# Kernel optimization log

Measured on AMD Instinct MI355X. Metric: run time of the kernel, lower is better.

The kernel has to match this reference:

```python
import jax, jax.numpy as jnp
import numpy as np

HID = 256      # cfg.MODEL.YOSO.HIDDEN_DIM
NPROP = 100    # cfg.MODEL.YOSO.NUM_PROPOSALS
K1 = 3         # CONV_KERNEL_SIZE_1D
K2 = 1         # CONV_KERNEL_SIZE_2D
NCLS = 80      # NUM_CLASSES
NHEAD = 8

def layernorm(x, g, b, eps=1e-5):
    m = jnp.mean(x, -1, keepdims=True)
    v = jnp.var(x, -1, keepdims=True)
    return (x - m) * jax.lax.rsqrt(v + eps) * g + b

def dysep(query, value, Wl, bl, ng, nb):
    # dynamic depthwise conv (kernel K1 along feature axis, one kernel per proposal)
    # followed by dynamic pointwise NxN conv, per torch F.conv1d semantics (cross-correlation, 'same' pad)
    w = query @ Wl + bl                      # [B,N,N+K1]
    dw = w[..., :K1]                         # [B,N,K1] depthwise kernels
    pw = w[..., K1:]                         # [B,N,N]  pointwise mixing
    C = value.shape[-1]
    pad = K1 // 2
    vp = jnp.pad(value, ((0, 0), (0, 0), (pad, pad)))
    depth = sum(dw[..., k:k + 1] * vp[..., k:k + C] for k in range(K1))
    depth = jax.nn.relu(depth)
    point = jnp.einsum('bmn,bnc->bmc', pw, depth)
    return layernorm(point, ng, nb)

def mha(x, in_w, in_b, out_w, out_b):
    B, N, E = x.shape
    d = E // NHEAD
    qkv = x @ in_w + in_b
    q, k, v = jnp.split(qkv, 3, axis=-1)
    q = q.reshape(B, N, NHEAD, d)
    k = k.reshape(B, N, NHEAD, d)
    v = v.reshape(B, N, NHEAD, d)
    att = jnp.einsum('bqhd,bkhd->bhqk', q, k) / jnp.sqrt(jnp.asarray(d, x.dtype))
    att = jax.nn.softmax(att, axis=-1)
    o = jnp.einsum('bhqk,bkhd->bqhd', att, v).reshape(B, N, E)
    return o @ out_w + out_b

def setup_inputs() -> dict:
    key = jax.random.key(0)
    ks = iter(jax.random.split(key, 64))
    B, H, W = 8, 128, 128
    E = HID * K2 * K2
    nrm = lambda *s: jax.random.normal(next(ks), s, jnp.float32) * 0.02
    bias_value = -np.log((1 - 0.01) / 0.01)
    return dict(
        features=jax.random.normal(next(ks), (B, HID, H, W), jnp.float32),
        proposal_kernels=jax.random.normal(next(ks), (B, NPROP, E), jnp.float32),
        mask_preds=jax.random.normal(next(ks), (B, NPROP, H, W), jnp.float32),
        fW=nrm(E, NPROP + K1), fb=jnp.zeros(NPROP + K1), fng=jnp.ones(E), fnb=jnp.zeros(E),
        f_norm_g=jnp.ones(E), f_norm_b=jnp.zeros(E),
        kW=nrm(E, NPROP + K1), kb=jnp.zeros(NPROP + K1), kng=jnp.ones(E), knb=jnp.zeros(E),
        k_norm_g=jnp.ones(E), k_norm_b=jnp.zeros(E),
        attn_in_w=nrm(E, 3 * E), attn_in_b=jnp.zeros(3 * E),
        attn_out_w=nrm(E, E), attn_out_b=jnp.zeros(E),
        s_norm_g=jnp.ones(E), s_norm_b=jnp.zeros(E),
        ffn_w1=nrm(HID, 2048), ffn_b1=jnp.zeros(2048),
        ffn_w2=nrm(2048, HID), ffn_b2=jnp.zeros(HID),
        ffn_norm_g=jnp.ones(HID), ffn_norm_b=jnp.zeros(HID),
        cls_w=nrm(HID, HID), cls_ln_g=jnp.ones(HID), cls_ln_b=jnp.zeros(HID),
        fc_cls_w=nrm(HID, NCLS + 1), fc_cls_b=jnp.full((NCLS + 1,), bias_value, jnp.float32),
        mask_w=nrm(3, HID, HID), mask_ln_g=jnp.ones((3, HID)), mask_ln_b=jnp.zeros((3, HID)),
        fc_mask_w=nrm(HID, HID), fc_mask_b=jnp.zeros(HID),
        train_flag=1,
    )

def reference(features, proposal_kernels, mask_preds, fW, fb, fng, fnb, f_norm_g, f_norm_b,
              kW, kb, kng, knb, k_norm_g, k_norm_b,
              attn_in_w, attn_in_b, attn_out_w, attn_out_b, s_norm_g, s_norm_b,
              ffn_w1, ffn_b1, ffn_w2, ffn_b2, ffn_norm_g, ffn_norm_b,
              cls_w, cls_ln_g, cls_ln_b, fc_cls_w, fc_cls_b,
              mask_w, mask_ln_g, mask_ln_b, fc_mask_w, fc_mask_b, train_flag):
    B, C, H, W = features.shape
    hard = (jax.nn.sigmoid(mask_preds) > 0.5).astype(features.dtype)   # hard masks (no grad path)
    f = jnp.einsum('bnhw,bchw->bnc', hard, features)                   # mask-pooled features [B,N,E]
    k = proposal_kernels.reshape(B, NPROP, -1)
    f = layernorm(f + dysep(k, f, fW, fb, fng, fnb), f_norm_g, f_norm_b)
    kk = layernorm(f + dysep(k, f, kW, kb, kng, knb), k_norm_g, k_norm_b)
    kk = layernorm(kk + mha(kk, attn_in_w, attn_in_b, attn_out_w, attn_out_b), s_norm_g, s_norm_b)
    obj = jnp.transpose(kk.reshape(B, NPROP, HID, -1), (0, 1, 3, 2))   # [B,N,K2*K2,HID]
    h = jax.nn.relu(obj @ ffn_w1 + ffn_b1)
    obj = layernorm(obj + (h @ ffn_w2 + ffn_b2), ffn_norm_g, ffn_norm_b)
    cls_feat = obj.sum(-2)                                             # [B,N,HID]
    mask_feat = obj
    if train_flag:
        cls_feat = jax.nn.relu(layernorm(cls_feat @ cls_w, cls_ln_g, cls_ln_b))
        cls_score = (cls_feat @ fc_cls_w + fc_cls_b).reshape(B, NPROP, -1)
    else:
        cls_score = None
    for i in range(mask_w.shape[0]):
        mask_feat = jax.nn.relu(layernorm(mask_feat @ mask_w[i], mask_ln_g[i], mask_ln_b[i]))
    mask_kernels = (mask_feat @ fc_mask_w + fc_mask_b)[:, :, 0, :]     # squeeze(2), K2*K2==1
    new_mask_preds = jnp.einsum('bqc,bchw->bqhw', mask_kernels, features)
    obj_out = jnp.transpose(obj, (0, 1, 3, 2)).reshape(B, NPROP, HID, K2, K2)
    return (cls_score, new_mask_preds, obj_out)
```

## Files before the change

kernel.cpp:

```cpp
#include <hip/hip_runtime.h>

typedef float f32x4 __attribute__((ext_vector_type(4)));
typedef short bfrag __attribute__((ext_vector_type(8)));
typedef short sh4 __attribute__((ext_vector_type(4)));

__device__ __forceinline__ unsigned short f2bf(float x) {
  unsigned int u = __float_as_uint(x);
  return (unsigned short)((u + 0x7FFFu + ((u >> 16) & 1u)) >> 16);
}
__device__ __forceinline__ float bf2f(unsigned short u) {
  return __uint_as_float(((unsigned int)u) << 16);
}
__device__ __forceinline__ float wred_sum(float v) {
#pragma unroll
  for (int o = 32; o > 0; o >>= 1) v += __shfl_xor(v, o);
  return v;
}
__device__ __forceinline__ float wred_max(float v) {
#pragma unroll
  for (int o = 32; o > 0; o >>= 1) v = fmaxf(v, __shfl_xor(v, o));
  return v;
}

struct Prep12 {
  const float* s[12];
  int K[12];
  int N[12];
  int base[12];
  int doff[12];
};

__global__ __launch_bounds__(256) void prep_w(Prep12 p, unsigned short* wt) {
  int t = blockIdx.x;
  int wi = 0;
#pragma unroll
  for (int i = 0; i < 11; ++i)
    if (t >= p.base[i + 1]) wi = i + 1;
  int lt = t - p.base[wi];
  int K = p.K[wi], N = p.N[wi];
  int tkn = (K + 31) >> 5;
  int tk = lt % tkn, tn = lt / tkn;
  __shared__ float tile[32][33];
  const float* src = p.s[wi];
#pragma unroll
  for (int i = 0; i < 4; ++i) {
    int flat = i * 256 + threadIdx.x;
    int kl = flat >> 5, nl = flat & 31;
    int k = tk * 32 + kl, n = tn * 32 + nl;
    tile[kl][nl] = (k < K && n < N) ? src[(size_t)k * N + n] : 0.f;
  }
  __syncthreads();
  unsigned short* dst = wt + p.doff[wi];
#pragma unroll
  for (int i = 0; i < 4; ++i) {
    int flat = i * 256 + threadIdx.x;
    int nl = flat >> 5, kl = flat & 31;
    int k = tk * 32 + kl, n = tn * 32 + nl;
    if (k < K && n < N) {
      int np = (wi < 2) ? ((n >= 3) ? n - 3 : n + 100) : n;
      dst[(size_t)np * K + k] = f2bf(tile[kl][nl]);
    }
  }
}

__global__ __launch_bounds__(256) void prep_bias(const float* __restrict__ fb_,
                                                 const float* __restrict__ kb_,
                                                 float* __restrict__ bf,
                                                 float* __restrict__ bk) {
  int t = threadIdx.x;
  if (t < 103) {
    int np = (t >= 3) ? t - 3 : t + 100;
    bf[np] = fb_[t];
    bk[np] = kb_[t];
  }
  if (t == 103) { bf[103] = 0.f; bk[103] = 0.f; }
}

template <int ABF, int OBF>
__global__ __launch_bounds__(256) void gemm_mf(const void* Av,
                                               const unsigned short* __restrict__ Wt,
                                               const float* __restrict__ bias,
                                               void* Cv, int M, int K, int N, int ldc, int relu) {
  __shared__ short Al[64 * 72];
  __shared__ short Wl[64 * 72];
  int tid = threadIdx.x;
  int r0 = blockIdx.x * 64;
  int c0 = blockIdx.y * 64;
  int w = tid >> 6, lane = tid & 63, quad = lane >> 4, l15 = lane & 15;

  f32x4 acc[4];
#pragma unroll
  for (int mt = 0; mt < 4; ++mt) {
    acc[mt][0] = 0.f; acc[mt][1] = 0.f; acc[mt][2] = 0.f; acc[mt][3] = 0.f;
  }

  for (int k0 = 0; k0 < K; k0 += 64) {
    if (ABF) {
      const unsigned short* A = (const unsigned short*)Av;
#pragma unroll
      for (int p = 0; p < 2; ++p) {
        int flat = p * 256 + tid;
        int row = flat >> 3, k8 = flat & 7;
        bfrag v;
        if (r0 + row < M)
          v = *(const bfrag*)(A + (size_t)(r0 + row) * K + k0 + k8 * 8);
        else
          v = (bfrag)(short)0;
        *(bfrag*)(Al + row * 72 + k8 * 8) = v;
      }
    } else {
      const float* A = (const float*)Av;
#pragma unroll
      for (int p = 0; p < 4; ++p) {
        int flat = p * 256 + tid;
        int row = flat >> 4, c4 = flat & 15;
        sh4 o4;
        if (r0 + row < M) {
          float4 v = *(const float4*)(A + (size_t)(r0 + row) * K + k0 + c4 * 4);
          o4[0] = (short)f2bf(v.x); o4[1] = (short)f2bf(v.y);
          o4[2] = (short)f2bf(v.z); o4[3] = (short)f2bf(v.w);
        } else {
          o4[0] = 0; o4[1] = 0; o4[2] = 0; o4[3] = 0;
        }
        *(sh4*)(Al + row * 72 + c4 * 4) = o4;
      }
    }
#pragma unroll
    for (int p = 0; p < 2; ++p) {
      int flat = p * 256 + tid;
      int row = flat >> 3, k8 = flat & 7;
      bfrag v;
      if (c0 + row < N)
        v = *(const bfrag*)(Wt + (size_t)(c0 + row) * K + k0 + k8 * 8);
      else
        v = (bfrag)(short)0;
      *(bfrag*)(Wl + row * 72 + k8 * 8) = v;
    }
    __syncthreads();
#pragma unroll
    for (int kk = 0; kk < 2; ++kk) {
      bfrag bv = *(const bfrag*)(Wl + (w * 16 + l15) * 72 + kk * 32 + quad * 8);
#pragma unroll
      for (int mt = 0; mt < 4; ++mt) {
        bfrag av = *(const bfrag*)(Al + (mt * 16 + l15) * 72 + kk * 32 + quad * 8);
        acc[mt] = __builtin_amdgcn_mfma_f32_16x16x32_bf16(av, bv, acc[mt], 0, 0, 0);
      }
    }
    __syncthreads();
  }
  int col = c0 + w * 16 + l15;
  if (col < N) {
    float bv = bias ? bias[col] : 0.f;
#pragma unroll
    for (int mt = 0; mt < 4; ++mt)
#pragma unroll
      for (int r = 0; r < 4; ++r) {
        int m = r0 + mt * 16 + quad * 4 + r;
        if (m < M) {
          float v = acc[mt][r] + bv;
          if (relu) v = fmaxf(v, 0.f);
          if (OBF)
            ((unsigned short*)Cv)[(size_t)m * ldc + col] = f2bf(v);
          else
            ((float*)Cv)[(size_t)m * ldc + col] = v;
        }
      }
  }
}

__global__ __launch_bounds__(512, 4) void phaseA(const float* __restrict__ mask,
                                                 const float* __restrict__ feat,
                                                 float* __restrict__ partial) {
  int tid = threadIdx.x;
  int ks = blockIdx.x;
  int ct = blockIdx.y;
  int b  = blockIdx.z;
  __shared__ short Al[2][112 * 72];
  __shared__ short Bl[2][128 * 72];
  int w = tid >> 6, lane = tid & 63, quad = lane >> 4, l15 = lane & 15;

  int rbase = tid >> 4;
  int c4 = tid & 15;
  const float* mrow = mask + (size_t)(b * 100 + rbase) * 16384 + c4 * 4;
  const float* frow = feat + (size_t)(b * 256 + ct * 128 + rbase) * 16384 + c4 * 4;

  f32x4 acc[7];
#pragma unroll
  for (int mt = 0; mt < 7; ++mt) {
    acc[mt][0] = 0.f; acc[mt][1] = 0.f; acc[mt][2] = 0.f; acc[mt][3] = 0.f;
  }

  for (int z = tid; z < 384; z += 512) {
    int bufi = z / 192, rem = z % 192;
    sh4 zz; zz[0] = 0; zz[1] = 0; zz[2] = 0; zz[3] = 0;
    *(sh4*)(&Al[bufi][(100 + (rem >> 4)) * 72 + (rem & 15) * 4]) = zz;
  }

  int k0 = ks * 512;
  {
    float4 apf[4], bpf[4];
#pragma unroll
    for (int p = 0; p < 4; ++p) {
      int row = rbase + 32 * p;
      if (row < 100) apf[p] = *(const float4*)(mrow + (size_t)p * 32 * 16384 + k0);
      bpf[p] = *(const float4*)(frow + (size_t)p * 32 * 16384 + k0);
    }
#pragma unroll
    for (int p = 0; p < 4; ++p) {
      int row = rbase + 32 * p;
      if (row < 100) {
        sh4 o4;
        o4[0] = (apf[p].x > 0.f) ? (short)0x3F80 : (short)0;
        o4[1] = (apf[p].y > 0.f) ? (short)0x3F80 : (short)0;
        o4[2] = (apf[p].z > 0.f) ? (short)0x3F80 : (short)0;
        o4[3] = (apf[p].w > 0.f) ? (short)0x3F80 : (short)0;
        *(sh4*)(&Al[0][row * 72 + c4 * 4]) = o4;
      }
      sh4 o4b;
      o4b[0] = (short)f2bf(bpf[p].x);
      o4b[1] = (short)f2bf(bpf[p].y);
      o4b[2] = (short)f2bf(bpf[p].z);
      o4b[3] = (short)f2bf(bpf[p].w);
      *(sh4*)(&Bl[0][row * 72 + c4 * 4]) = o4b;
    }
  }
  __syncthreads();

  int cur = 0;
  for (int st = 0; st < 8; ++st) {
    float4 apf[4], bpf[4];
    if (st < 7) {
      int kb = k0 + (st + 1) * 64;
#pragma unroll
      for (int p = 0; p < 4; ++p) {
        int row = rbase + 32 * p;
        if (row < 100) apf[p] = *(const float4*)(mrow + (size_t)p * 32 * 16384 + kb);
        bpf[p] = *(const float4*)(frow + (size_t)p * 32 * 16384 + kb);
      }
    }
#pragma unroll
    for (int kk = 0; kk < 2; ++kk) {
      bfrag bv = *(const bfrag*)(&Bl[cur][(w * 16 + l15) * 72 + kk * 32 + quad * 8]);
#pragma unroll
      for (int mt = 0; mt < 7; ++mt) {
        bfrag av = *(const bfrag*)(&Al[cur][(mt * 16 + l15) * 72 + kk * 32 + quad * 8]);
        acc[mt] = __builtin_amdgcn_mfma_f32_16x16x32_bf16(av, bv, acc[mt], 0, 0, 0);
      }
    }
    __builtin_amdgcn_sched_barrier(0);
    if (st < 7) {
      int nxt = cur ^ 1;
#pragma unroll
      for (int p = 0; p < 4; ++p) {
        int row = rbase + 32 * p;
        if (row < 100) {
          sh4 o4;
          o4[0] = (apf[p].x > 0.f) ? (short)0x3F80 : (short)0;
          o4[1] = (apf[p].y > 0.f) ? (short)0x3F80 : (short)0;
          o4[2] = (apf[p].z > 0.f) ? (short)0x3F80 : (short)0;
          o4[3] = (apf[p].w > 0.f) ? (short)0x3F80 : (short)0;
          *(sh4*)(&Al[nxt][row * 72 + c4 * 4]) = o4;
        }
        sh4 o4b;
        o4b[0] = (short)f2bf(bpf[p].x);
        o4b[1] = (short)f2bf(bpf[p].y);
        o4b[2] = (short)f2bf(bpf[p].z);
        o4b[3] = (short)f2bf(bpf[p].w);
        *(sh4*)(&Bl[nxt][row * 72 + c4 * 4]) = o4b;
      }
    }
    __syncthreads();
    cur ^= 1;
  }

  float* pb = partial + (size_t)(b * 32 + ks) * (100 * 256) + ct * 128 + w * 16 + l15;
#pragma unroll
  for (int mt = 0; mt < 7; ++mt)
#pragma unroll
    for (int r = 0; r < 4; ++r) {
      int m = mt * 16 + quad * 4 + r;
      if (m < 100) pb[(size_t)m * 256] = acc[mt][r];
    }
}

__global__ __launch_bounds__(256) void reduceA(const float* __restrict__ partial,
                                               float* __restrict__ fm) {
  int gid = blockIdx.x * 256 + threadIdx.x;
  int c = gid & 255, row = gid >> 8;
  int b = row / 100, n = row % 100;
  float s = 0.f;
#pragma unroll
  for (int ks = 0; ks < 32; ++ks)
    s += partial[((size_t)(b * 32 + ks) * 100 + n) * 256 + c];
  fm[(size_t)row * 256 + c] = s;
}

__global__ __launch_bounds__(256) void pointdw(const float* __restrict__ fm,
                                               const float* __restrict__ wbuf,
                                               float* __restrict__ point) {
  int tid = threadIdx.x;
  int b = blockIdx.y, c0 = blockIdx.x * 32;
  __shared__ float dl[100 * 33];
  for (int flat = tid; flat < 3200; flat += 256) {
    int n = flat >> 5, cl = flat & 31, c = c0 + cl;
    const float* fr = fm + (size_t)(b * 100 + n) * 256;
    const float* wr = wbuf + (size_t)(b * 100 + n) * 104;
    float x0 = (c > 0) ? fr[c - 1] : 0.f;
    float x1 = fr[c];
    float x2 = (c < 255) ? fr[c + 1] : 0.f;
    float d = wr[100] * x0 + wr[101] * x1 + wr[102] * x2;
    dl[n * 33 + cl] = fmaxf(d, 0.f);
  }
  __syncthreads();
  int cl = tid & 31, mg = tid >> 5;
  for (int m = mg; m < 100; m += 8) {
    const float4* pw4 = (const float4*)(wbuf + (size_t)(b * 100 + m) * 104);
    float a = 0.f;
#pragma unroll
    for (int n4 = 0; n4 < 25; ++n4) {
      float4 wv = pw4[n4];
      a += wv.x * dl[(n4 * 4 + 0) * 33 + cl] + wv.y * dl[(n4 * 4 + 1) * 33 + cl]
         + wv.z * dl[(n4 * 4 + 2) * 33 + cl] + wv.w * dl[(n4 * 4 + 3) * 33 + cl];
    }
    point[(size_t)(b * 100 + m) * 256 + c0 + cl] = a;
  }
}

__global__ __launch_bounds__(256) void ln2_kernel(const float* __restrict__ x,
                                                  const float* __restrict__ resid,
                                                  const float* __restrict__ g1, const float* __restrict__ b1,
                                                  const float* __restrict__ g2, const float* __restrict__ b2,
                                                  float* __restrict__ out) {
  int tid = threadIdx.x;
  int row = blockIdx.x * 4 + (tid >> 6);
  int lane = tid & 63;
  size_t base = (size_t)row * 256 + lane * 4;
  float4 v = *(const float4*)(x + base);
  float mean = wred_sum(v.x + v.y + v.z + v.w) * (1.f / 256.f);
  float d0 = v.x - mean, d1 = v.y - mean, d2 = v.z - mean, d3 = v.w - mean;
  float rs = rsqrtf(wred_sum(d0 * d0 + d1 * d1 + d2 * d2 + d3 * d3) * (1.f / 256.f) + 1e-5f);
  float4 gv = *(const float4*)(g1 + lane * 4);
  float4 bv = *(const float4*)(b1 + lane * 4);
  float4 rv = *(const float4*)(resid + base);
  float y0 = rv.x + d0 * rs * gv.x + bv.x;
  float y1 = rv.y + d1 * rs * gv.y + bv.y;
  float y2 = rv.z + d2 * rs * gv.z + bv.z;
  float y3 = rv.w + d3 * rs * gv.w + bv.w;
  float mean2 = wred_sum(y0 + y1 + y2 + y3) * (1.f / 256.f);
  float e0 = y0 - mean2, e1 = y1 - mean2, e2 = y2 - mean2, e3 = y3 - mean2;
  float rs2 = rsqrtf(wred_sum(e0 * e0 + e1 * e1 + e2 * e2 + e3 * e3) * (1.f / 256.f) + 1e-5f);
  float4 g2v = *(const float4*)(g2 + lane * 4);
  float4 b2v = *(const float4*)(b2 + lane * 4);
  float4 o;
  o.x = e0 * rs2 * g2v.x + b2v.x;
  o.y = e1 * rs2 * g2v.y + b2v.y;
  o.z = e2 * rs2 * g2v.z + b2v.z;
  o.w = e3 * rs2 * g2v.w + b2v.w;
  *(float4*)(out + base) = o;
}

__global__ __launch_bounds__(256) void ln_kernel(const float* __restrict__ x,
                                                 const float* __restrict__ res,
                                                 const float* __restrict__ g, const float* __restrict__ bb,
                                                 float* __restrict__ out, int relu,
                                                 float* __restrict__ copy2) {
  int tid = threadIdx.x;
  int row = blockIdx.x * 4 + (tid >> 6);
  int lane = tid & 63;
  size_t base = (size_t)row * 256 + lane * 4;
  float4 v = *(const float4*)(x + base);
  if (res) {
    float4 rv = *(const float4*)(res + base);
    v.x += rv.x; v.y += rv.y; v.z += rv.z; v.w += rv.w;
  }
  float mean = wred_sum(v.x + v.y + v.z + v.w) * (1.f / 256.f);
  float d0 = v.x - mean, d1 = v.y - mean, d2 = v.z - mean, d3 = v.w - mean;
  float rs = rsqrtf(wred_sum(d0 * d0 + d1 * d1 + d2 * d2 + d3 * d3) * (1.f / 256.f) + 1e-5f);
  float4 gv = *(const float4*)(g + lane * 4);
  float4 bv = *(const float4*)(bb + lane * 4);
  float4 o;
  o.x = d0 * rs * gv.x + bv.x;
  o.y = d1 * rs * gv.y + bv.y;
  o.z = d2 * rs * gv.z + bv.z;
  o.w = d3 * rs * gv.w + bv.w;
  if (relu) {
    o.x = fmaxf(o.x, 0.f); o.y = fmaxf(o.y, 0.f);
    o.z = fmaxf(o.z, 0.f); o.w = fmaxf(o.w, 0.f);
  }
  *(float4*)(out + base) = o;
  if (copy2) *(float4*)(copy2 + base) = o;
}

__global__ __launch_bounds__(256) void attn_kernel(const float* __restrict__ qkv,
                                                   float* __restrict__ obuf) {
  int tid = threadIdx.x;
  int b = blockIdx.y, h = blockIdx.x;
  __shared__ float ktj[100 * 32];
  __shared__ unsigned short vl[100 * 32];
  __shared__ float sl[100 * 100];
  const float* base = qkv + (size_t)b * 100 * 768;
  for (int flat = tid; flat < 3200; flat += 256) {
    int j = flat >> 5, dd = flat & 31;
    ktj[j * 32 + dd] = base[(size_t)j * 768 + 256 + h * 32 + dd];
    vl[j * 32 + dd] = f2bf(base[(size_t)j * 768 + 512 + h * 32 + dd]);
  }
  __syncthreads();
  {
    int i = tid >> 1;
    int jh = (tid & 1) * 50;
    int qi = (i < 100) ? i : 0;
    const float4* q4 = (const float4*)(base + (size_t)qi * 768 + h * 32);
    float4 q[8];
#pragma unroll
    for (int d4 = 0; d4 < 8; ++d4) q[d4] = q4[d4];
    if (i < 100) {
      for (int jj = 0; jj < 50; ++jj) {
        int j = jh + jj;
        const float4* kr = (const float4*)(ktj + j * 32);
        float a = 0.f;
#pragma unroll
        for (int d4 = 0; d4 < 8; ++d4) {
          float4 kv = kr[d4];
          a += q[d4].x * kv.x + q[d4].y * kv.y + q[d4].z * kv.z + q[d4].w * kv.w;
        }
        sl[i * 100 + j] = a * 0.17677669529663687f;
      }
    }
  }
  __syncthreads();
  int w = tid >> 6, lane = tid & 63;
  for (int r = w; r < 100; r += 4) {
    float x0 = sl[r * 100 + lane];
    float x1 = (lane + 64 < 100) ? sl[r * 100 + lane + 64] : -1e30f;
    float mx = wred_max(fmaxf(x0, x1));
    float e0 = __expf(x0 - mx);
    float e1 = (lane + 64 < 100) ? __expf(x1 - mx) : 0.f;
    float inv = 1.f / wred_sum(e0 + e1);
    sl[r * 100 + lane] = e0 * inv;
    if (lane + 64 < 100) sl[r * 100 + lane + 64] = e1 * inv;
  }
  __syncthreads();
  for (int flat = tid; flat < 3200; flat += 256) {
    int i = flat >> 5, dd = flat & 31;
    float a = 0.f;
#pragma unroll 4
    for (int j = 0; j < 100; ++j) a += sl[i * 100 + j] * bf2f(vl[j * 32 + dd]);
    obuf[(size_t)(b * 100 + i) * 256 + h * 32 + dd] = a;
  }
}

__global__ __launch_bounds__(256) void phaseE(const float* __restrict__ mk,
                                              const float* __restrict__ feat,
                                              float* __restrict__ out) {
  int tid = threadIdx.x;
  int b = blockIdx.y;
  int hw0 = blockIdx.x * 128;
  __shared__ short Al[112 * 264];
#pragma unroll
  for (int p = 0; p < 28; ++p) {
    int flat = p * 256 + tid;
    int row = flat >> 6, c4 = flat & 63;
    sh4 o4;
    if (row < 100) {
      float4 v = *(const float4*)(mk + (size_t)(b * 100 + row) * 256 + c4 * 4);
      o4[0] = (short)f2bf(v.x); o4[1] = (short)f2bf(v.y);
      o4[2] = (short)f2bf(v.z); o4[3] = (short)f2bf(v.w);
    } else {
      o4[0] = 0; o4[1] = 0; o4[2] = 0; o4[3] = 0;
    }
    *(sh4*)(Al + row * 264 + c4 * 4) = o4;
  }
  __syncthreads();
  int w = tid >> 6, lane = tid & 63, quad = lane >> 4, l15 = lane & 15;
  f32x4 acc[7][2];
#pragma unroll
  for (int mt = 0; mt < 7; ++mt)
#pragma unroll
    for (int nt = 0; nt < 2; ++nt) {
      acc[mt][nt][0] = 0.f; acc[mt][nt][1] = 0.f; acc[mt][nt][2] = 0.f; acc[mt][nt][3] = 0.f;
    }
  size_t fb = (size_t)b * 256 * 16384;
  int hwl = hw0 + w * 32 + l15;
  for (int kk = 0; kk < 8; ++kk) {
    bfrag bv[2];
#pragma unroll
    for (int nt = 0; nt < 2; ++nt) {
#pragma unroll
      for (int j = 0; j < 8; ++j) {
        float v = feat[fb + (size_t)(kk * 32 + quad * 8 + j) * 16384 + hwl + nt * 16];
        bv[nt][j] = (short)f2bf(v);
      }
    }
    bfrag av[7];
#pragma unroll
    for (int mt = 0; mt < 7; ++mt)
      av[mt] = *(const bfrag*)(Al + (mt * 16 + l15) * 264 + kk * 32 + quad * 8);
#pragma unroll
    for (int mt = 0; mt < 7; ++mt) {
      acc[mt][0] = __builtin_amdgcn_mfma_f32_16x16x32_bf16(av[mt], bv[0], acc[mt][0], 0, 0, 0);
      acc[mt][1] = __builtin_amdgcn_mfma_f32_16x16x32_bf16(av[mt], bv[1], acc[mt][1], 0, 0, 0);
    }
  }
#pragma unroll
  for (int mt = 0; mt < 7; ++mt)
#pragma unroll
    for (int nt = 0; nt < 2; ++nt)
#pragma unroll
      for (int r = 0; r < 4; ++r) {
        int m = mt * 16 + quad * 4 + r;
        if (m < 100)
          out[(size_t)(b * 100 + m) * 16384 + hw0 + w * 32 + nt * 16 + l15] = acc[mt][nt][r];
      }
}

extern "C" void kernel_launch(void* const* d_in, const int* in_sizes, int n_in,
                              void* d_out, int out_size, void* d_ws, size_t ws_size,
                              hipStream_t stream) {
  const float* feat    = (const float*)d_in[0];
  const float* prop    = (const float*)d_in[1];
  const float* maskp   = (const float*)d_in[2];
  const float* fW      = (const float*)d_in[3];
  const float* fb_     = (const float*)d_in[4];
  const float* fng     = (const float*)d_in[5];
  const float* fnb     = (const float*)d_in[6];
  const float* f_ng    = (const float*)d_in[7];
  const float* f_nb    = (const float*)d_in[8];
  const float* kW      = (const float*)d_in[9];
  const float* kb_     = (const float*)d_in[10];
  const float* kng     = (const float*)d_in[11];
  const float* knb     = (const float*)d_in[12];
  const float* k_ng    = (const float*)d_in[13];
  const float* k_nb    = (const float*)d_in[14];
  const float* aw_in   = (const float*)d_in[15];
  const float* ab_in   = (const float*)d_in[16];
  const float* aw_out  = (const float*)d_in[17];
  const float* ab_out  = (const float*)d_in[18];
  const float* s_ng    = (const float*)d_in[19];
  const float* s_nb    = (const float*)d_in[20];
  const float* w1      = (const float*)d_in[21];
  const float* b1      = (const float*)d_in[22];
  const float* w2      = (const float*)d_in[23];
  const float* b2      = (const float*)d_in[24];
  const float* ffn_ng  = (const float*)d_in[25];
  const float* ffn_nb  = (const float*)d_in[26];
  const float* cls_w   = (const float*)d_in[27];
  const float* cls_g   = (const float*)d_in[28];
  const float* cls_b   = (const float*)d_in[29];
  const float* fcclsw  = (const float*)d_in[30];
  const float* fcclsb  = (const float*)d_in[31];
  const float* mask_w  = (const float*)d_in[32];
  const float* mask_g  = (const float*)d_in[33];
  const float* mask_b  = (const float*)d_in[34];
  const float* fcmw    = (const float*)d_in[35];
  const float* fcmb    = (const float*)d_in[36];
  float* out = (float*)d_out;

  float* ws = (float*)d_ws;
  size_t off = 0;
  unsigned short* wt = (unsigned short*)(ws + off); off += 856192;
  float* fm     = ws + off; off += 204800;
  float* bias_f = ws + off; off += 104;
  float* bias_k = ws + off; off += 104;
  float* partial = ws + off;
  float* ub = partial;
  size_t uo = 0;
  float* wb   = ub + uo; uo += 83200;
  float* pt   = ub + uo; uo += 204800;
  float* fbuf = ub + uo; uo += 204800;
  float* kkb  = ub + uo; uo += 204800;
  float* qkvb = ub + uo; uo += 614400;
  float* ob   = ub + uo; uo += 204800;
  float* mo   = ub + uo; uo += 204800;
  float* kk2  = ub + uo; uo += 204800;
  float* t1   = ub + uo; uo += 204800;
  float* objb = ub + uo; uo += 204800;
  float* t2   = ub + uo; uo += 204800;
  float* mkb  = ub + uo; uo += 204800;
  unsigned short* ffn1b = (unsigned short*)(ub + uo); uo += 409600;

  const int wt_fW = 0, wt_kW = 26624, wt_ain = 53248, wt_aout = 249856;
  const int wt_w1 = 315392, wt_w2 = 839680, wt_cls = 1363968, wt_fccls = 1429504;
  const int wt_m0 = 1450240, wt_m1 = 1515776, wt_m2 = 1581312, wt_fcm = 1646848;

  float* out_cls  = out;
  float* out_mask = out + 64800;
  float* out_obj  = out + 64800 + 13107200;

  Prep12 p;
  const float* srcs[12] = {fW, kW, aw_in, aw_out, w1, w2, cls_w, fcclsw,
                           mask_w, mask_w + 65536, mask_w + 131072, fcmw};
  int Ks[12]    = {256, 256, 256, 256, 256, 2048, 256, 256, 256, 256, 256, 256};
  int Ns[12]    = {103, 103, 768, 256, 2048, 256, 256, 81, 256, 256, 256, 256};
  int doffs[12] = {wt_fW, wt_kW, wt_ain, wt_aout, wt_w1, wt_w2, wt_cls, wt_fccls,
                   wt_m0, wt_m1, wt_m2, wt_fcm};
  int tb = 0;
  for (int i = 0; i < 12; ++i) {
    p.s[i] = srcs[i]; p.K[i] = Ks[i]; p.N[i] = Ns[i]; p.doff[i] = doffs[i];
    p.base[i] = tb;
    tb += ((Ks[i] + 31) / 32) * ((Ns[i] + 31) / 32);
  }
  prep_w<<<tb, 256, 0, stream>>>(p, wt);
  prep_bias<<<1, 256, 0, stream>>>(fb_, kb_, bias_f, bias_k);

  phaseA<<<dim3(32, 2, 8), 512, 0, stream>>>(maskp, feat, partial);
  reduceA<<<800, 256, 0, stream>>>(partial, fm);
  gemm_mf<0, 0><<<dim3(13, 2), 256, 0, stream>>>(prop, wt + wt_fW, bias_f, wb, 800, 256, 103, 104, 0);
  pointdw<<<dim3(8, 8), 256, 0, stream>>>(fm, wb, pt);
  ln2_kernel<<<200, 256, 0, stream>>>(pt, fm, fng, fnb, f_ng, f_nb, fbuf);
  gemm_mf<0, 0><<<dim3(13, 2), 256, 0, stream>>>(prop, wt + wt_kW, bias_k, wb, 800, 256, 103, 104, 0);
  pointdw<<<dim3(8, 8), 256, 0, stream>>>(fbuf, wb, pt);
  ln2_kernel<<<200, 256, 0, stream>>>(pt, fbuf, kng, knb, k_ng, k_nb, kkb);
  gemm_mf<0, 0><<<dim3(13, 12), 256, 0, stream>>>(kkb, wt + wt_ain, ab_in, qkvb, 800, 256, 768, 768, 0);
  attn_kernel<<<dim3(8, 8), 256, 0, stream>>>(qkvb, ob);
  gemm_mf<0, 0><<<dim3(13, 4), 256, 0, stream>>>(ob, wt + wt_aout, ab_out, mo, 800, 256, 256, 256, 0);
  ln_kernel<<<200, 256, 0, stream>>>(mo, kkb, s_ng, s_nb, kk2, 0, nullptr);
  gemm_mf<0, 1><<<dim3(13, 32), 256, 0, stream>>>(kk2, wt + wt_w1, b1, ffn1b, 800, 256, 2048, 2048, 1);
  gemm_mf<1, 0><<<dim3(13, 4), 256, 0, stream>>>(ffn1b, wt + wt_w2, b2, t1, 800, 2048, 256, 256, 0);
  ln_kernel<<<200, 256, 0, stream>>>(t1, kk2, ffn_ng, ffn_nb, objb, 0, out_obj);
  gemm_mf<0, 0><<<dim3(13, 4), 256, 0, stream>>>(objb, wt + wt_cls, nullptr, t1, 800, 256, 256, 256, 0);
  ln_kernel<<<200, 256, 0, stream>>>(t1, nullptr, cls_g, cls_b, t2, 1, nullptr);
  gemm_mf<0, 0><<<dim3(13, 2), 256, 0, stream>>>(t2, wt + wt_fccls, fcclsb, out_cls, 800, 256, 81, 81, 0);
  gemm_mf<0, 0><<<dim3(13, 4), 256, 0, stream>>>(objb, wt + wt_m0, nullptr, t1, 800, 256, 256, 256, 0);
  ln_kernel<<<200, 256, 0, stream>>>(t1, nullptr, mask_g, mask_b, t2, 1, nullptr);
  gemm_mf<0, 0><<<dim3(13, 4), 256, 0, stream>>>(t2, wt + wt_m1, nullptr, t1, 800, 256, 256, 256, 0);
  ln_kernel<<<200, 256, 0, stream>>>(t1, nullptr, mask_g + 256, mask_b + 256, t2, 1, nullptr);
  gemm_mf<0, 0><<<dim3(13, 4), 256, 0, stream>>>(t2, wt + wt_m2, nullptr, t1, 800, 256, 256, 256, 0);
  ln_kernel<<<200, 256, 0, stream>>>(t1, nullptr, mask_g + 512, mask_b + 512, t2, 1, nullptr);
  gemm_mf<0, 0><<<dim3(13, 4), 256, 0, stream>>>(t2, wt + wt_fcm, fcmb, mkb, 800, 256, 256, 256, 0);
  phaseE<<<dim3(128, 8), 256, 0, stream>>>(mkb, feat, out_mask);
}
```

Before: 680.5 us.

## Pack mask signs to bits, fuse classification/mask head, stream bf16 kernels in phaseE

A new pre-pass packs the binarized mask predictions into bitmasks, so phaseA reads 1 bit per element instead of a float, cutting its mask traffic. The chain of head GEMMs and layernorms (cls and the three mask layers plus fc_mask) is fused into one fp32 CUDA-core kernel with one wave per row, which removes about ten launches and the weight prep for those matrices. phaseE now reads bf16 mask kernels straight from global memory instead of staging them in LDS. The costs are an extra pass over the 52 MB mask tensor in pack_bits, scalar fp32 matmuls in place of MFMA, and no LDS reuse of the A operand in phaseE.

```diff
diff --git a/kernel.cpp b/kernel.cpp
--- a/kernel.cpp
+++ b/kernel.cpp
@@ -22,19 +22,19 @@
   return v;
 }
 
-struct Prep12 {
-  const float* s[12];
-  int K[12];
-  int N[12];
-  int base[12];
-  int doff[12];
+struct Prep6 {
+  const float* s[6];
+  int K[6];
+  int N[6];
+  int base[6];
+  int doff[6];
 };
 
-__global__ __launch_bounds__(256) void prep_w(Prep12 p, unsigned short* wt) {
+__global__ __launch_bounds__(256) void prep_w(Prep6 p, unsigned short* wt) {
   int t = blockIdx.x;
   int wi = 0;
 #pragma unroll
-  for (int i = 0; i < 11; ++i)
+  for (int i = 0; i < 5; ++i)
     if (t >= p.base[i + 1]) wi = i + 1;
   int lt = t - p.base[wi];
   int K = p.K[wi], N = p.N[wi];
@@ -74,6 +74,20 @@
     bk[np] = kb_[t];
   }
   if (t == 103) { bf[103] = 0.f; bk[103] = 0.f; }
+}
+
+__global__ __launch_bounds__(256) void pack_bits(const float* __restrict__ mask,
+                                                 unsigned int* __restrict__ bits) {
+  int tid = threadIdx.x;
+  size_t f = (size_t)blockIdx.x * 256 + tid;
+  float4 m = *(const float4*)(mask + f * 4);
+  unsigned int n = (m.x > 0.f ? 1u : 0u) | (m.y > 0.f ? 2u : 0u) |
+                   (m.z > 0.f ? 4u : 0u) | (m.w > 0.f ? 8u : 0u);
+  n <<= ((tid & 7) * 4);
+  n |= (unsigned int)__shfl_xor((int)n, 1);
+  n |= (unsigned int)__shfl_xor((int)n, 2);
+  n |= (unsigned int)__shfl_xor((int)n, 4);
+  if ((tid & 7) == 0) bits[((size_t)blockIdx.x * 32) + (tid >> 3)] = n;
 }
 
 template <int ABF, int OBF>
@@ -168,7 +182,7 @@
   }
 }
 
-__global__ __launch_bounds__(512, 4) void phaseA(const float* __restrict__ mask,
+__global__ __launch_bounds__(512, 4) void phaseA(const unsigned int* __restrict__ bits,
                                                  const float* __restrict__ feat,
                                                  float* __restrict__ partial) {
   int tid = threadIdx.x;
@@ -181,8 +195,11 @@
 
   int rbase = tid >> 4;
   int c4 = tid & 15;
-  const float* mrow = mask + (size_t)(b * 100 + rbase) * 16384 + c4 * 4;
   const float* frow = feat + (size_t)(b * 256 + ct * 128 + rbase) * 16384 + c4 * 4;
+
+  int arow = tid >> 2, q = tid & 3;
+  bool aact = tid < 400;
+  const unsigned int* brow = bits + (size_t)(b * 100 + arow) * 512 + (q >> 1);
 
   f32x4 acc[7];
 #pragma unroll
@@ -198,24 +215,15 @@
 
   int k0 = ks * 512;
   {
-    float4 apf[4], bpf[4];
+    float4 bpf[4];
+    unsigned int awd = 0;
+#pragma unroll
+    for (int p = 0; p < 4; ++p)
+      bpf[p] = *(const float4*)(frow + (size_t)p * 32 * 16384 + k0);
+    if (aact) awd = brow[k0 >> 5];
 #pragma unroll
     for (int p = 0; p < 4; ++p) {
       int row = rbase + 32 * p;
-      if (row < 100) apf[p] = *(const float4*)(mrow + (size_t)p * 32 * 16384 + k0);
-      bpf[p] = *(const float4*)(frow + (size_t)p * 32 * 16384 + k0);
-    }
-#pragma unroll
-    for (int p = 0; p < 4; ++p) {
-      int row = rbase + 32 * p;
-      if (row < 100) {
-        sh4 o4;
-        o4[0] = (apf[p].x > 0.f) ? (short)0x3F80 : (short)0;
-        o4[1] = (apf[p].y > 0.f) ? (short)0x3F80 : (short)0;
-        o4[2] = (apf[p].z > 0.f) ? (short)0x3F80 : (short)0;
-        o4[3] = (apf[p].w > 0.f) ? (short)0x3F80 : (short)0;
-        *(sh4*)(&Al[0][row * 72 + c4 * 4]) = o4;
-      }
       sh4 o4b;
       o4b[0] = (short)f2bf(bpf[p].x);
       o4b[1] = (short)f2bf(bpf[p].y);
@@ -223,20 +231,29 @@
       o4b[3] = (short)f2bf(bpf[p].w);
       *(sh4*)(&Bl[0][row * 72 + c4 * 4]) = o4b;
     }
+    if (aact) {
+      unsigned int hw16 = (awd >> ((q & 1) * 16)) & 0xFFFFu;
+      bfrag e0, e1;
+#pragma unroll
+      for (int i = 0; i < 8; ++i) e0[i] = ((hw16 >> i) & 1u) ? (short)0x3F80 : (short)0;
+#pragma unroll
+      for (int i = 0; i < 8; ++i) e1[i] = ((hw16 >> (i + 8)) & 1u) ? (short)0x3F80 : (short)0;
+      *(bfrag*)(&Al[0][arow * 72 + q * 16]) = e0;
+      *(bfrag*)(&Al[0][arow * 72 + q * 16 + 8]) = e1;
+    }
   }
   __syncthreads();
 
   int cur = 0;
   for (int st = 0; st < 8; ++st) {
-    float4 apf[4], bpf[4];
+    float4 bpf[4];
+    unsigned int awd = 0;
     if (st < 7) {
       int kb = k0 + (st + 1) * 64;
 #pragma unroll
-      for (int p = 0; p < 4; ++p) {
-        int row = rbase + 32 * p;
-        if (row < 100) apf[p] = *(const float4*)(mrow + (size_t)p * 32 * 16384 + kb);
+      for (int p = 0; p < 4; ++p)
         bpf[p] = *(const float4*)(frow + (size_t)p * 32 * 16384 + kb);
-      }
+      if (aact) awd = brow[kb >> 5];
     }
 #pragma unroll
     for (int kk = 0; kk < 2; ++kk) {
@@ -253,20 +270,22 @@
 #pragma unroll
       for (int p = 0; p < 4; ++p) {
         int row = rbase + 32 * p;
-        if (row < 100) {
-          sh4 o4;
-          o4[0] = (apf[p].x > 0.f) ? (short)0x3F80 : (short)0;
-          o4[1] = (apf[p].y > 0.f) ? (short)0x3F80 : (short)0;
-          o4[2] = (apf[p].z > 0.f) ? (short)0x3F80 : (short)0;
-          o4[3] = (apf[p].w > 0.f) ? (short)0x3F80 : (short)0;
-          *(sh4*)(&Al[nxt][row * 72 + c4 * 4]) = o4;
-        }
         sh4 o4b;
         o4b[0] = (short)f2bf(bpf[p].x);
         o4b[1] = (short)f2bf(bpf[p].y);
         o4b[2] = (short)f2bf(bpf[p].z);
         o4b[3] = (short)f2bf(bpf[p].w);
         *(sh4*)(&Bl[nxt][row * 72 + c4 * 4]) = o4b;
+      }
+      if (aact) {
+        unsigned int hw16 = (awd >> ((q & 1) * 16)) & 0xFFFFu;
+        bfrag e0, e1;
+#pragma unroll
+        for (int i = 0; i < 8; ++i) e0[i] = ((hw16 >> i) & 1u) ? (short)0x3F80 : (short)0;
+#pragma unroll
+        for (int i = 0; i < 8; ++i) e1[i] = ((hw16 >> (i + 8)) & 1u) ? (short)0x3F80 : (short)0;
+        *(bfrag*)(&Al[nxt][arow * 72 + q * 16]) = e0;
+        *(bfrag*)(&Al[nxt][arow * 72 + q * 16 + 8]) = e1;
       }
     }
     __syncthreads();
@@ -449,28 +468,93 @@
   }
 }
 
-__global__ __launch_bounds__(256) void phaseE(const float* __restrict__ mk,
-                                              const float* __restrict__ feat,
-                                              float* __restrict__ out) {
+__global__ __launch_bounds__(256) void head_fused(
+    const float* __restrict__ objb,
+    const float* __restrict__ cls_w, const float* __restrict__ cls_g, const float* __restrict__ cls_b,
+    const float* __restrict__ fcclsw, const float* __restrict__ fcclsb,
+    const float* __restrict__ mask_w, const float* __restrict__ mask_g, const float* __restrict__ mask_b,
+    const float* __restrict__ fcmw, const float* __restrict__ fcmb,
+    float* __restrict__ out_cls, unsigned short* __restrict__ mk16) {
+  int tid = threadIdx.x, wv = tid >> 6, lane = tid & 63;
+  int row = blockIdx.x * 4 + wv;
+  __shared__ float xs[4][260];
+  __shared__ float x0[4][260];
+  {
+    float4 v = *(const float4*)(objb + (size_t)row * 256 + lane * 4);
+    *(float4*)(&x0[wv][lane * 4]) = v;
+    *(float4*)(&xs[wv][lane * 4]) = v;
+  }
+  for (int li = 0; li < 3; ++li) {
+    const float* W = mask_w + li * 65536;
+    float a0 = 0.f, a1 = 0.f, a2 = 0.f, a3 = 0.f;
+#pragma unroll 4
+    for (int k = 0; k < 256; ++k) {
+      float xk = xs[wv][k];
+      float4 wvv = *(const float4*)(W + (size_t)k * 256 + lane * 4);
+      a0 += xk * wvv.x; a1 += xk * wvv.y; a2 += xk * wvv.z; a3 += xk * wvv.w;
+    }
+    float mean = wred_sum(a0 + a1 + a2 + a3) * (1.f / 256.f);
+    float d0 = a0 - mean, d1 = a1 - mean, d2 = a2 - mean, d3 = a3 - mean;
+    float rs = rsqrtf(wred_sum(d0 * d0 + d1 * d1 + d2 * d2 + d3 * d3) * (1.f / 256.f) + 1e-5f);
+    float4 gv = *(const float4*)(mask_g + li * 256 + lane * 4);
+    float4 bv = *(const float4*)(mask_b + li * 256 + lane * 4);
+    float y0 = fmaxf(d0 * rs * gv.x + bv.x, 0.f);
+    float y1 = fmaxf(d1 * rs * gv.y + bv.y, 0.f);
+    float y2 = fmaxf(d2 * rs * gv.z + bv.z, 0.f);
+    float y3 = fmaxf(d3 * rs * gv.w + bv.w, 0.f);
+    float4 o; o.x = y0; o.y = y1; o.z = y2; o.w = y3;
+    *(float4*)(&xs[wv][lane * 4]) = o;
+  }
+  {
+    float a0 = 0.f, a1 = 0.f, a2 = 0.f, a3 = 0.f;
+#pragma unroll 4
+    for (int k = 0; k < 256; ++k) {
+      float xk = xs[wv][k];
+      float4 wvv = *(const float4*)(fcmw + (size_t)k * 256 + lane * 4);
+      a0 += xk * wvv.x; a1 += xk * wvv.y; a2 += xk * wvv.z; a3 += xk * wvv.w;
+    }
+    float4 bv = *(const float4*)(fcmb + lane * 4);
+    sh4 o;
+    o[0] = (short)f2bf(a0 + bv.x); o[1] = (short)f2bf(a1 + bv.y);
+    o[2] = (short)f2bf(a2 + bv.z); o[3] = (short)f2bf(a3 + bv.w);
+    *(sh4*)(mk16 + (size_t)row * 256 + lane * 4) = o;
+  }
+  {
+    float a0 = 0.f, a1 = 0.f, a2 = 0.f, a3 = 0.f;
+#pragma unroll 4
+    for (int k = 0; k < 256; ++k) {
+      float xk = x0[wv][k];
+      float4 wvv = *(const float4*)(cls_w + (size_t)k * 256 + lane * 4);
+      a0 += xk * wvv.x; a1 += xk * wvv.y; a2 += xk * wvv.z; a3 += xk * wvv.w;
+    }
+    float mean = wred_sum(a0 + a1 + a2 + a3) * (1.f / 256.f);
+    float d0 = a0 - mean, d1 = a1 - mean, d2 = a2 - mean, d3 = a3 - mean;
+    float rs = rsqrtf(wred_sum(d0 * d0 + d1 * d1 + d2 * d2 + d3 * d3) * (1.f / 256.f) + 1e-5f);
+    float4 gv = *(const float4*)(cls_g + lane * 4);
+    float4 bv = *(const float4*)(cls_b + lane * 4);
+    float4 o;
+    o.x = fmaxf(d0 * rs * gv.x + bv.x, 0.f);
+    o.y = fmaxf(d1 * rs * gv.y + bv.y, 0.f);
+    o.z = fmaxf(d2 * rs * gv.z + bv.z, 0.f);
+    o.w = fmaxf(d3 * rs * gv.w + bv.w, 0.f);
+    *(float4*)(&xs[wv][lane * 4]) = o;
+    float c0 = 0.f, c1 = 0.f;
+    for (int k = 0; k < 256; ++k) {
+      float xk = xs[wv][k];
+      c0 += xk * fcclsw[(size_t)k * 81 + lane];
+      if (lane < 17) c1 += xk * fcclsw[(size_t)k * 81 + 64 + lane];
+    }
+    out_cls[(size_t)row * 81 + lane] = c0 + fcclsb[lane];
+    if (lane < 17) out_cls[(size_t)row * 81 + 64 + lane] = c1 + fcclsb[64 + lane];
+  }
+}
+
+__global__ __launch_bounds__(256, 4) void phaseE(const unsigned short* __restrict__ mk16,
+                                                 const float* __restrict__ feat,
+                                                 float* __restrict__ out) {
   int tid = threadIdx.x;
   int b = blockIdx.y;
   int hw0 = blockIdx.x * 128;
-  __shared__ short Al[112 * 264];
-#pragma unroll
-  for (int p = 0; p < 28; ++p) {
-    int flat = p * 256 + tid;
-    int row = flat >> 6, c4 = flat & 63;
-    sh4 o4;
-    if (row < 100) {
-      float4 v = *(const float4*)(mk + (size_t)(b * 100 + row) * 256 + c4 * 4);
-      o4[0] = (short)f2bf(v.x); o4[1] = (short)f2bf(v.y);
-      o4[2] = (short)f2bf(v.z); o4[3] = (short)f2bf(v.w);
-    } else {
-      o4[0] = 0; o4[1] = 0; o4[2] = 0; o4[3] = 0;
-    }
-    *(sh4*)(Al + row * 264 + c4 * 4) = o4;
-  }
-  __syncthreads();
   int w = tid >> 6, lane = tid & 63, quad = lane >> 4, l15 = lane & 15;
   f32x4 acc[7][2];
 #pragma unroll
@@ -481,6 +565,7 @@
     }
   size_t fb = (size_t)b * 256 * 16384;
   int hwl = hw0 + w * 32 + l15;
+  const unsigned short* mkb_b = mk16 + (size_t)b * 100 * 256;
   for (int kk = 0; kk < 8; ++kk) {
     bfrag bv[2];
 #pragma unroll
@@ -493,8 +578,11 @@
     }
     bfrag av[7];
 #pragma unroll
-    for (int mt = 0; mt < 7; ++mt)
-      av[mt] = *(const bfrag*)(Al + (mt * 16 + l15) * 264 + kk * 32 + quad * 8);
+    for (int mt = 0; mt < 7; ++mt) {
+      int row = mt * 16 + l15;
+      int rr = (row < 100) ? row : 0;
+      av[mt] = *(const bfrag*)(mkb_b + (size_t)rr * 256 + kk * 32 + quad * 8);
+    }
 #pragma unroll
     for (int mt = 0; mt < 7; ++mt) {
       acc[mt][0] = __builtin_amdgcn_mfma_f32_16x16x32_bf16(av[mt], bv[0], acc[mt][0], 0, 0, 0);
@@ -557,10 +645,11 @@
 
   float* ws = (float*)d_ws;
   size_t off = 0;
-  unsigned short* wt = (unsigned short*)(ws + off); off += 856192;
+  unsigned short* wt = (unsigned short*)(ws + off); off += 681984;
   float* fm     = ws + off; off += 204800;
   float* bias_f = ws + off; off += 104;
   float* bias_k = ws + off; off += 104;
+  unsigned int* bitsbuf = (unsigned int*)(ws + off); off += 409600;
   float* partial = ws + off;
   float* ub = partial;
   size_t uo = 0;
@@ -574,35 +663,33 @@
   float* kk2  = ub + uo; uo += 204800;
   float* t1   = ub + uo; uo += 204800;
   float* objb = ub + uo; uo += 204800;
-  float* t2   = ub + uo; uo += 204800;
   float* mkb  = ub + uo; uo += 204800;
   unsigned short* ffn1b = (unsigned short*)(ub + uo); uo += 409600;
+  unsigned short* mkb16 = (unsigned short*)mkb;
 
   const int wt_fW = 0, wt_kW = 26624, wt_ain = 53248, wt_aout = 249856;
-  const int wt_w1 = 315392, wt_w2 = 839680, wt_cls = 1363968, wt_fccls = 1429504;
-  const int wt_m0 = 1450240, wt_m1 = 1515776, wt_m2 = 1581312, wt_fcm = 1646848;
+  const int wt_w1 = 315392, wt_w2 = 839680;
 
   float* out_cls  = out;
   float* out_mask = out + 64800;
   float* out_obj  = out + 64800 + 13107200;
 
-  Prep12 p;
-  const float* srcs[12] = {fW, kW, aw_in, aw_out, w1, w2, cls_w, fcclsw,
-                           mask_w, mask_w + 65536, mask_w + 131072, fcmw};
-  int Ks[12]    = {256, 256, 256, 256, 256, 2048, 256, 256, 256, 256, 256, 256};
-  int Ns[12]    = {103, 103, 768, 256, 2048, 256, 256, 81, 256, 256, 256, 256};
-  int doffs[12] = {wt_fW, wt_kW, wt_ain, wt_aout, wt_w1, wt_w2, wt_cls, wt_fccls,
-                   wt_m0, wt_m1, wt_m2, wt_fcm};
+  Prep6 p;
+  const float* srcs[6] = {fW, kW, aw_in, aw_out, w1, w2};
+  int Ks[6]    = {256, 256, 256, 256, 256, 2048};
+  int Ns[6]    = {103, 103, 768, 256, 2048, 256};
+  int doffs[6] = {wt_fW, wt_kW, wt_ain, wt_aout, wt_w1, wt_w2};
   int tb = 0;
-  for (int i = 0; i < 12; ++i) {
+  for (int i = 0; i < 6; ++i) {
     p.s[i] = srcs[i]; p.K[i] = Ks[i]; p.N[i] = Ns[i]; p.doff[i] = doffs[i];
     p.base[i] = tb;
     tb += ((Ks[i] + 31) / 32) * ((Ns[i] + 31) / 32);
   }
   prep_w<<<tb, 256, 0, stream>>>(p, wt);
   prep_bias<<<1, 256, 0, stream>>>(fb_, kb_, bias_f, bias_k);
-
-  phaseA<<<dim3(32, 2, 8), 512, 0, stream>>>(maskp, feat, partial);
+  pack_bits<<<12800, 256, 0, stream>>>(maskp, bitsbuf);
+
+  phaseA<<<dim3(32, 2, 8), 512, 0, stream>>>(bitsbuf, feat, partial);
   reduceA<<<800, 256, 0, stream>>>(partial, fm);
   gemm_mf<0, 0><<<dim3(13, 2), 256, 0, stream>>>(prop, wt + wt_fW, bias_f, wb, 800, 256, 103, 104, 0);
   pointdw<<<dim3(8, 8), 256, 0, stream>>>(fm, wb, pt);
@@ -617,15 +704,8 @@
   gemm_mf<0, 1><<<dim3(13, 32), 256, 0, stream>>>(kk2, wt + wt_w1, b1, ffn1b, 800, 256, 2048, 2048, 1);
   gemm_mf<1, 0><<<dim3(13, 4), 256, 0, stream>>>(ffn1b, wt + wt_w2, b2, t1, 800, 2048, 256, 256, 0);
   ln_kernel<<<200, 256, 0, stream>>>(t1, kk2, ffn_ng, ffn_nb, objb, 0, out_obj);
-  gemm_mf<0, 0><<<dim3(13, 4), 256, 0, stream>>>(objb, wt + wt_cls, nullptr, t1, 800, 256, 256, 256, 0);
-  ln_kernel<<<200, 256, 0, stream>>>(t1, nullptr, cls_g, cls_b, t2, 1, nullptr);
-  gemm_mf<0, 0><<<dim3(13, 2), 256, 0, stream>>>(t2, wt + wt_fccls, fcclsb, out_cls, 800, 256, 81, 81, 0);
-  gemm_mf<0, 0><<<dim3(13, 4), 256, 0, stream>>>(objb, wt + wt_m0, nullptr, t1, 800, 256, 256, 256, 0);
-  ln_kernel<<<200, 256, 0, stream>>>(t1, nullptr, mask_g, mask_b, t2, 1, nullptr);
-  gemm_mf<0, 0><<<dim3(13, 4), 256, 0, stream>>>(t2, wt + wt_m1, nullptr, t1, 800, 256, 256, 256, 0);
-  ln_kernel<<<200, 256, 0, stream>>>(t1, nullptr, mask_g + 256, mask_b + 256, t2, 1, nullptr);
-  gemm_mf<0, 0><<<dim3(13, 4), 256, 0, stream>>>(t2, wt + wt_m2, nullptr, t1, 800, 256, 256, 256, 0);
-  ln_kernel<<<200, 256, 0, stream>>>(t1, nullptr, mask_g + 512, mask_b + 512, t2, 1, nullptr);
-  gemm_mf<0, 0><<<dim3(13, 4), 256, 0, stream>>>(t2, wt + wt_fcm, fcmb, mkb, 800, 256, 256, 256, 0);
-  phaseE<<<dim3(128, 8), 256, 0, stream>>>(mkb, feat, out_mask);
-}
+  head_fused<<<200, 256, 0, stream>>>(objb, cls_w, cls_g, cls_b, fcclsw, fcclsb,
+                                      mask_w, mask_g, mask_b, fcmw, fcmb,
+                                      out_cls, mkb16);
+  phaseE<<<dim3(128, 8), 256, 0, stream>>>(mkb16, feat, out_mask);
+}
```

New measurement: 847.7 us. +24.6%, slower.
